# Performance work log

Measured on AMD Instinct MI355X. Metric: run time of the kernel, lower is better.

## Reference

```python
import jax, jax.numpy as jnp
import numpy as np

N_NODES = 100000
N_EDGES = 3200000
N_FEAT = 512
N_GRAPHS = 64
N_EXTRA_LAYERS = 3  # layers 2..4, all 1->1


def setup_inputs() -> dict:
    key = jax.random.key(0)
    ks = jax.random.split(key, 10)
    x = jax.random.normal(ks[0], (N_NODES, N_FEAT), dtype=jnp.float32)
    edge_src = jax.random.randint(ks[1], (N_EDGES,), 0, N_NODES, dtype=jnp.int32)
    edge_dst = jax.random.randint(ks[2], (N_EDGES,), 0, N_NODES, dtype=jnp.int32)
    graph_ids = jnp.sort(jax.random.randint(ks[3], (N_NODES,), 0, N_GRAPHS, dtype=jnp.int32))
    W_neigh0 = jax.random.normal(ks[4], (N_FEAT, 1), dtype=jnp.float32) * 0.05
    W_self0 = jax.random.normal(ks[5], (N_FEAT, 1), dtype=jnp.float32) * 0.05
    b0 = jax.random.normal(ks[6], (1,), dtype=jnp.float32)
    W_neigh_r = jax.random.normal(ks[7], (N_EXTRA_LAYERS, 1, 1), dtype=jnp.float32)
    W_self_r = jax.random.normal(ks[8], (N_EXTRA_LAYERS, 1, 1), dtype=jnp.float32)
    b_r = jax.random.normal(ks[9], (N_EXTRA_LAYERS, 1), dtype=jnp.float32)
    return {"x": x, "edge_src": edge_src, "edge_dst": edge_dst, "graph_ids": graph_ids,
            "W_neigh0": W_neigh0, "W_self0": W_self0, "b0": b0,
            "W_neigh_r": W_neigh_r, "W_self_r": W_self_r, "b_r": b_r}


def _conv_wl(h, edge_src, edge_dst, W_neigh, W_self, b, n_nodes):
    # GraphConv(norm='none'): project first (in >= out here), gather at src, scatter-sum at dst, + bias
    proj = h @ W_neigh                      # [N, out]
    neigh = jax.ops.segment_sum(proj[edge_src], edge_dst, num_segments=n_nodes) + b
    return neigh + h @ W_self               # residual self-loop linear (no bias)


def reference(x, edge_src, edge_dst, graph_ids, W_neigh0, W_self0, b0, W_neigh_r, W_self_r, b_r):
    n = x.shape[0]
    xs = [x]
    h = jax.nn.relu(_conv_wl(x, edge_src, edge_dst, W_neigh0, W_self0, b0, n))
    xs.append(h)
    for i in range(W_neigh_r.shape[0]):
        h = jax.nn.relu(_conv_wl(h, edge_src, edge_dst, W_neigh_r[i], W_self_r[i], b_r[i], n))
        xs.append(h)
    hcat = jnp.concatenate(xs, axis=1)       # [N, F + num_layers] (concat_features=True)
    # dgl.sum_nodes: per-graph sum over the batched graph
    return jax.ops.segment_sum(hcat, graph_ids, num_segments=N_GRAPHS)  # [G, F + L]
```

## Files before the change

kernel.cpp:

```cpp
#include <hip/hip_runtime.h>

#define N_NODES  100000
#define N_EDGES  3200000
#define N_FEAT   512
#define N_GRAPHS 64
#define N_COLS   516
#define NBINS    1563
#define B1       256
#define EPB      (N_EDGES / B1)
#define CCHUNK   16
#define SRC_MASK 0x1FFFF

__global__ __launch_bounds__(256) void find_starts_kernel(
    const int* __restrict__ gid, int* __restrict__ starts)
{
    const int n = blockIdx.x * blockDim.x + threadIdx.x;
    if (n >= N_NODES) return;
    const int g = gid[n];
    const int gp = (n == 0) ? -1 : gid[n - 1];
    for (int q = gp + 1; q <= g; ++q) starts[q] = n;
    if (n == N_NODES - 1)
        for (int q = g + 1; q <= N_GRAPHS; ++q) starts[q] = N_NODES;
}

__global__ __launch_bounds__(256) void dots_kernel(
    const float* __restrict__ x, const float* __restrict__ wn,
    const float* __restrict__ ws, float* __restrict__ p0, float* __restrict__ s0)
{
    const int lane = threadIdx.x & 63;
    const int wid = (blockIdx.x * blockDim.x + threadIdx.x) >> 6;
    const int nwaves = (gridDim.x * blockDim.x) >> 6;

    const float4 wna = *(const float4*)(wn + lane * 8);
    const float4 wnb = *(const float4*)(wn + lane * 8 + 4);
    const float4 wsa = *(const float4*)(ws + lane * 8);
    const float4 wsb = *(const float4*)(ws + lane * 8 + 4);

    for (int n = wid; n < N_NODES; n += nwaves) {
        const float* row = x + (size_t)n * N_FEAT;
        const float4 xa = *(const float4*)(row + lane * 8);
        const float4 xb = *(const float4*)(row + lane * 8 + 4);
        float dn = xa.x*wna.x + xa.y*wna.y + xa.z*wna.z + xa.w*wna.w
                 + xb.x*wnb.x + xb.y*wnb.y + xb.z*wnb.z + xb.w*wnb.w;
        float dv = xa.x*wsa.x + xa.y*wsa.y + xa.z*wsa.z + xa.w*wsa.w
                 + xb.x*wsb.x + xb.y*wsb.y + xb.z*wsb.z + xb.w*wsb.w;
        #pragma unroll
        for (int off = 32; off > 0; off >>= 1) {
            dn += __shfl_down(dn, off);
            dv += __shfl_down(dv, off);
        }
        if (lane == 0) { p0[n] = dn; s0[n] = dv; }
    }
}

__global__ __launch_bounds__(256) void colsum_kernel(
    const float* __restrict__ x, const int* __restrict__ starts,
    float* __restrict__ partial)
{
    const int g = blockIdx.y, chunk = blockIdx.x;
    const int walker = threadIdx.x >> 7;
    const int t = threadIdx.x & 127;
    const int s = starts[g], e = starts[g + 1];
    const int len = e - s;
    const int rs = s + (int)(((long long)len * chunk) / CCHUNK);
    const int re = s + (int)(((long long)len * (chunk + 1)) / CCHUNK);

    float4 acc = make_float4(0.f, 0.f, 0.f, 0.f);
    for (int r = rs + walker; r < re; r += 2) {
        const float4 v = *(const float4*)(x + (size_t)r * N_FEAT + t * 4);
        acc.x += v.x; acc.y += v.y; acc.z += v.z; acc.w += v.w;
    }
    const int slot = chunk * 2 + walker;
    *(float4*)(partial + ((size_t)slot * N_GRAPHS + g) * N_FEAT + t * 4) = acc;
}

__global__ __launch_bounds__(512) void reduce_partial_kernel(
    const float* __restrict__ partial, float* __restrict__ out)
{
    const int g = blockIdx.x, c = threadIdx.x;
    float s = 0.f;
    for (int k = 0; k < 2 * CCHUNK; ++k)
        s += partial[((size_t)k * N_GRAPHS + g) * N_FEAT + c];
    out[(size_t)g * N_COLS + c] = s;
}

__global__ __launch_bounds__(256) void hist_kernel(
    const int* __restrict__ edst, int* __restrict__ histG)
{
    __shared__ int lh[NBINS];
    const int b = blockIdx.x, tid = threadIdx.x;
    for (int i = tid; i < NBINS; i += 256) lh[i] = 0;
    __syncthreads();
    const int e0 = b * EPB;
    for (int e = e0 + tid; e < e0 + EPB; e += 256)
        atomicAdd(&lh[edst[e] >> 6], 1);
    __syncthreads();
    for (int i = tid; i < NBINS; i += 256) histG[i * B1 + b] = lh[i];
}

__global__ __launch_bounds__(256) void colscan_kernel(
    const int* __restrict__ histG, int* __restrict__ colscanG,
    int* __restrict__ totalG)
{
    __shared__ int sc[256];
    const int bin = blockIdx.x, t = threadIdx.x;
    const int v = histG[bin * B1 + t];
    sc[t] = v;
    __syncthreads();
    for (int off = 1; off < 256; off <<= 1) {
        const int a = (t >= off) ? sc[t - off] : 0;
        __syncthreads();
        sc[t] += a;
        __syncthreads();
    }
    colscanG[bin * B1 + t] = sc[t] - v;
    if (t == 255) totalG[bin] = sc[255];
}

__global__ __launch_bounds__(256) void scan2_kernel(
    const int* __restrict__ totalG, int* __restrict__ binstart)
{
    __shared__ int sc[256];
    const int t = threadIdx.x;
    const int CH = 7;
    int loc[CH];
    int s = 0;
    for (int i = 0; i < CH; ++i) {
        const int bin = t * CH + i;
        const int v = (bin < NBINS) ? totalG[bin] : 0;
        loc[i] = s; s += v;
    }
    const int my = s;
    sc[t] = my;
    __syncthreads();
    for (int off = 1; off < 256; off <<= 1) {
        const int a = (t >= off) ? sc[t - off] : 0;
        __syncthreads();
        sc[t] += a;
        __syncthreads();
    }
    const int texcl = sc[t] - my;
    for (int i = 0; i < CH; ++i) {
        const int bin = t * CH + i;
        if (bin < NBINS) binstart[bin] = texcl + loc[i];
    }
    if (t == 255) binstart[NBINS] = sc[255];
}

__global__ __launch_bounds__(256) void reorder_kernel(
    const int* __restrict__ esrc, const int* __restrict__ edst,
    const int* __restrict__ binstart, const int* __restrict__ colscanG,
    int* __restrict__ sorted)
{
    __shared__ int offs[NBINS];
    const int b = blockIdx.x, tid = threadIdx.x;
    for (int i = tid; i < NBINS; i += 256)
        offs[i] = binstart[i] + colscanG[i * B1 + b];
    __syncthreads();
    const int e0 = b * EPB;
    for (int e = e0 + tid; e < e0 + EPB; e += 256) {
        const int s = esrc[e], d = edst[e];
        const int p = atomicAdd(&offs[d >> 6], 1);
        sorted[p] = s | ((d & 63) << 17);
    }
}

__global__ __launch_bounds__(256) void binned_scatter_kernel(
    const int* __restrict__ sorted, const int* __restrict__ binstart,
    const float* __restrict__ pin, const float* __restrict__ self_in,
    const float* __restrict__ wself_p, const float* __restrict__ bias_p,
    const float* __restrict__ wnext_p,
    float* __restrict__ h_out, float* __restrict__ p_next,
    const int* __restrict__ gid, float* __restrict__ out, int col)
{
    __shared__ float acc[4][64];
    const int b = blockIdx.x, tid = threadIdx.x;
    ((float*)acc)[tid] = 0.f;
    __syncthreads();

    const int st = binstart[b], en = binstart[b + 1];
    const int w = tid >> 6;
    for (int e = st + tid; e < en; e += 256) {
        const int v = sorted[e];
        atomicAdd(&acc[w][v >> 17], pin[v & SRC_MASK]);
    }
    __syncthreads();

    if (tid < 64) {
        const int n = b * 64 + tid;
        const bool valid = (n < N_NODES);
        float h = 0.f;
        int g = 0;
        if (valid) {
            const float nb = acc[0][tid] + acc[1][tid] + acc[2][tid] + acc[3][tid];
            const float sw = wself_p ? *wself_p : 1.0f;
            const float v = nb + *bias_p + sw * self_in[n];
            h = v > 0.f ? v : 0.f;
            h_out[n] = h;
            if (wnext_p) p_next[n] = h * (*wnext_p);
            g = gid[n];
        }
        const int g0 = __shfl(g, 0);
        if (__all(!valid || g == g0)) {
            float s = h;
            #pragma unroll
            for (int off = 32; off > 0; off >>= 1) s += __shfl_down(s, off);
            if (tid == 0) atomicAdd(&out[(size_t)g0 * N_COLS + col], s);
        } else if (valid) {
            atomicAdd(&out[(size_t)g * N_COLS + col], h);
        }
    }
}

extern "C" void kernel_launch(void* const* d_in, const int* in_sizes, int n_in,
                              void* d_out, int out_size, void* d_ws, size_t ws_size,
                              hipStream_t stream)
{
    (void)in_sizes; (void)n_in; (void)out_size; (void)ws_size;

    const float* x    = (const float*)d_in[0];
    const int*   esrc = (const int*)d_in[1];
    const int*   edst = (const int*)d_in[2];
    const int*   gid  = (const int*)d_in[3];
    const float* Wn0  = (const float*)d_in[4];
    const float* Ws0  = (const float*)d_in[5];
    const float* b0p  = (const float*)d_in[6];
    const float* Wnr  = (const float*)d_in[7];
    const float* Wsr  = (const float*)d_in[8];
    const float* brp  = (const float*)d_in[9];
    float* out = (float*)d_out;

    float* bufP  = (float*)d_ws;
    float* bufP2 = bufP  + N_NODES;
    float* bufS  = bufP2 + N_NODES;
    float* bufH  = bufS  + N_NODES;
    int*   starts   = (int*)(bufH + N_NODES);
    int*   binstart = starts + (N_GRAPHS + 1);
    int*   totalG   = binstart + NBINS + 1;
    int*   histG    = totalG + NBINS;
    int*   colscanG = histG + (size_t)NBINS * B1;
    int*   sorted   = colscanG + (size_t)NBINS * B1;
    float* partial  = (float*)(sorted + N_EDGES);

    hipMemsetAsync(d_out, 0, (size_t)N_GRAPHS * N_COLS * sizeof(float), stream);

    find_starts_kernel<<<(N_NODES + 255) / 256, 256, 0, stream>>>(gid, starts);
    dots_kernel<<<1024, 256, 0, stream>>>(x, Wn0, Ws0, bufP, bufS);
    colsum_kernel<<<dim3(CCHUNK, N_GRAPHS), 256, 0, stream>>>(x, starts, partial);
    reduce_partial_kernel<<<N_GRAPHS, 512, 0, stream>>>(partial, out);

    hist_kernel<<<B1, 256, 0, stream>>>(edst, histG);
    colscan_kernel<<<NBINS, 256, 0, stream>>>(histG, colscanG, totalG);
    scan2_kernel<<<1, 256, 0, stream>>>(totalG, binstart);
    reorder_kernel<<<B1, 256, 0, stream>>>(esrc, edst, binstart, colscanG, sorted);

    binned_scatter_kernel<<<NBINS, 256, 0, stream>>>(
        sorted, binstart, bufP, bufS, nullptr, b0p, Wnr + 0, bufH, bufP2, gid, out, 512);
    binned_scatter_kernel<<<NBINS, 256, 0, stream>>>(
        sorted, binstart, bufP2, bufH, Wsr + 0, brp + 0, Wnr + 1, bufH, bufP, gid, out, 513);
    binned_scatter_kernel<<<NBINS, 256, 0, stream>>>(
        sorted, binstart, bufP, bufH, Wsr + 1, brp + 1, Wnr + 2, bufH, bufP2, gid, out, 514);
    binned_scatter_kernel<<<NBINS, 256, 0, stream>>>(
        sorted, binstart, bufP2, bufH, Wsr + 2, brp + 2, nullptr, bufH, nullptr, gid, out, 515);
}
```

Baseline: 525.6 us.

## Fuse x dot products with per-graph column sums in one pass over x

```diff
diff --git a/kernel.cpp b/kernel.cpp
--- a/kernel.cpp
+++ b/kernel.cpp
@@ -8,38 +8,93 @@
 #define NBINS    1563
 #define B1       256
 #define EPB      (N_EDGES / B1)
-#define CCHUNK   16
+#define CHUNK    25
+#define NWAVES   (N_NODES / CHUNK)
 #define SRC_MASK 0x1FFFF
 
-__global__ __launch_bounds__(256) void find_starts_kernel(
-    const int* __restrict__ gid, int* __restrict__ starts)
-{
-    const int n = blockIdx.x * blockDim.x + threadIdx.x;
-    if (n >= N_NODES) return;
-    const int g = gid[n];
-    const int gp = (n == 0) ? -1 : gid[n - 1];
-    for (int q = gp + 1; q <= g; ++q) starts[q] = n;
-    if (n == N_NODES - 1)
-        for (int q = g + 1; q <= N_GRAPHS; ++q) starts[q] = N_NODES;
-}
-
-__global__ __launch_bounds__(256) void dots_kernel(
-    const float* __restrict__ x, const float* __restrict__ wn,
-    const float* __restrict__ ws, float* __restrict__ p0, float* __restrict__ s0)
-{
+__global__ __launch_bounds__(1024) void prep_kernel(
+    const int* __restrict__ edst, const int* __restrict__ gid,
+    int* __restrict__ histG, int* __restrict__ starts, float* __restrict__ outz)
+{
+    __shared__ int lh[NBINS];
+    const int b = blockIdx.x, tid = threadIdx.x;
+    const int gtid = b * 1024 + tid;
+
+    if (gtid < N_GRAPHS * N_COLS) outz[gtid] = 0.f;
+    if (gtid < N_NODES) {
+        const int g = gid[gtid];
+        const int gp = gtid ? gid[gtid - 1] : -1;
+        for (int q = gp + 1; q <= g; ++q) starts[q] = gtid;
+        if (gtid == N_NODES - 1)
+            for (int q = g + 1; q <= N_GRAPHS; ++q) starts[q] = N_NODES;
+    }
+    for (int i = tid; i < NBINS; i += 1024) lh[i] = 0;
+    __syncthreads();
+    const int e0 = b * EPB;
+    for (int e = e0 + tid; e < e0 + EPB; e += 1024)
+        atomicAdd(&lh[edst[e] >> 6], 1);
+    __syncthreads();
+    for (int i = tid; i < NBINS; i += 1024) histG[i * B1 + b] = lh[i];
+}
+
+__device__ __forceinline__ void flush_cs(
+    int si, int cur_g, const float a[8], int wave, int lane,
+    float* __restrict__ pp, int* __restrict__ pt, float* __restrict__ out)
+{
+    if (si < 2) {
+        const int slot = wave * 2 + si;
+        if (lane == 0) pt[slot] = cur_g;
+        float* d = pp + (size_t)slot * N_FEAT + lane * 8;
+        *(float4*)d       = make_float4(a[0], a[1], a[2], a[3]);
+        *(float4*)(d + 4) = make_float4(a[4], a[5], a[6], a[7]);
+    } else {
+        float* o = out + (size_t)cur_g * N_COLS + lane * 8;
+        #pragma unroll
+        for (int k = 0; k < 8; ++k) atomicAdd(o + k, a[k]);
+    }
+}
+
+__global__ __launch_bounds__(256) void pass_x_kernel(
+    const float* __restrict__ x, const int* __restrict__ gid,
+    const float* __restrict__ wn, const float* __restrict__ ws,
+    float* __restrict__ p0, float* __restrict__ s0,
+    float* __restrict__ neigh, float* __restrict__ out,
+    float* __restrict__ pp, int* __restrict__ pt)
+{
+    const int wave = (blockIdx.x * blockDim.x + threadIdx.x) >> 6;
     const int lane = threadIdx.x & 63;
-    const int wid = (blockIdx.x * blockDim.x + threadIdx.x) >> 6;
-    const int nwaves = (gridDim.x * blockDim.x) >> 6;
+    const int start = wave * CHUNK, end = start + CHUNK;
+
+    for (int n = start + lane; n < end; n += 64) neigh[n] = 0.f;
 
     const float4 wna = *(const float4*)(wn + lane * 8);
     const float4 wnb = *(const float4*)(wn + lane * 8 + 4);
     const float4 wsa = *(const float4*)(ws + lane * 8);
     const float4 wsb = *(const float4*)(ws + lane * 8 + 4);
 
-    for (int n = wid; n < N_NODES; n += nwaves) {
+    float a[8] = {0.f, 0.f, 0.f, 0.f, 0.f, 0.f, 0.f, 0.f};
+    int cur_g = gid[start];
+    const bool uniform = (gid[end - 1] == cur_g);
+    int si = 0;
+
+    for (int n = start; n < end; ++n) {
+        if (!uniform) {
+            const int g = gid[n];
+            if (g != cur_g) {
+                flush_cs(si, cur_g, a, wave, lane, pp, pt, out);
+                ++si;
+                #pragma unroll
+                for (int k = 0; k < 8; ++k) a[k] = 0.f;
+                cur_g = g;
+            }
+        }
         const float* row = x + (size_t)n * N_FEAT;
         const float4 xa = *(const float4*)(row + lane * 8);
         const float4 xb = *(const float4*)(row + lane * 8 + 4);
+
+        a[0] += xa.x; a[1] += xa.y; a[2] += xa.z; a[3] += xa.w;
+        a[4] += xb.x; a[5] += xb.y; a[6] += xb.z; a[7] += xb.w;
+
         float dn = xa.x*wna.x + xa.y*wna.y + xa.z*wna.z + xa.w*wna.w
                  + xb.x*wnb.x + xb.y*wnb.y + xb.z*wnb.z + xb.w*wnb.w;
         float dv = xa.x*wsa.x + xa.y*wsa.y + xa.z*wsa.z + xa.w*wsa.w
@@ -51,51 +106,30 @@
         }
         if (lane == 0) { p0[n] = dn; s0[n] = dv; }
     }
-}
-
-__global__ __launch_bounds__(256) void colsum_kernel(
-    const float* __restrict__ x, const int* __restrict__ starts,
-    float* __restrict__ partial)
-{
-    const int g = blockIdx.y, chunk = blockIdx.x;
-    const int walker = threadIdx.x >> 7;
-    const int t = threadIdx.x & 127;
+    flush_cs(si, cur_g, a, wave, lane, pp, pt, out);
+    ++si;
+    if (lane == 0)
+        for (int s2 = si; s2 < 2; ++s2) pt[wave * 2 + s2] = -1;
+}
+
+__global__ __launch_bounds__(512) void reduce_x_kernel(
+    const float* __restrict__ pp, const int* __restrict__ pt,
+    const int* __restrict__ starts, float* __restrict__ out)
+{
+    const int g = blockIdx.x, c = threadIdx.x;
     const int s = starts[g], e = starts[g + 1];
-    const int len = e - s;
-    const int rs = s + (int)(((long long)len * chunk) / CCHUNK);
-    const int re = s + (int)(((long long)len * (chunk + 1)) / CCHUNK);
-
-    float4 acc = make_float4(0.f, 0.f, 0.f, 0.f);
-    for (int r = rs + walker; r < re; r += 2) {
-        const float4 v = *(const float4*)(x + (size_t)r * N_FEAT + t * 4);
-        acc.x += v.x; acc.y += v.y; acc.z += v.z; acc.w += v.w;
-    }
-    const int slot = chunk * 2 + walker;
-    *(float4*)(partial + ((size_t)slot * N_GRAPHS + g) * N_FEAT + t * 4) = acc;
-}
-
-__global__ __launch_bounds__(512) void reduce_partial_kernel(
-    const float* __restrict__ partial, float* __restrict__ out)
-{
-    const int g = blockIdx.x, c = threadIdx.x;
-    float s = 0.f;
-    for (int k = 0; k < 2 * CCHUNK; ++k)
-        s += partial[((size_t)k * N_GRAPHS + g) * N_FEAT + c];
-    out[(size_t)g * N_COLS + c] = s;
-}
-
-__global__ __launch_bounds__(256) void hist_kernel(
-    const int* __restrict__ edst, int* __restrict__ histG)
-{
-    __shared__ int lh[NBINS];
-    const int b = blockIdx.x, tid = threadIdx.x;
-    for (int i = tid; i < NBINS; i += 256) lh[i] = 0;
-    __syncthreads();
-    const int e0 = b * EPB;
-    for (int e = e0 + tid; e < e0 + EPB; e += 256)
-        atomicAdd(&lh[edst[e] >> 6], 1);
-    __syncthreads();
-    for (int i = tid; i < NBINS; i += 256) histG[i * B1 + b] = lh[i];
+    float acc = 0.f;
+    if (e > s) {
+        const int w0 = s / CHUNK, w1 = (e - 1) / CHUNK;
+        for (int w = w0; w <= w1; ++w) {
+            #pragma unroll
+            for (int k = 0; k < 2; ++k) {
+                const int slot = w * 2 + k;
+                if (pt[slot] == g) acc += pp[(size_t)slot * N_FEAT + c];
+            }
+        }
+    }
+    out[(size_t)g * N_COLS + c] += acc;
 }
 
 __global__ __launch_bounds__(256) void colscan_kernel(
@@ -147,18 +181,18 @@
     if (t == 255) binstart[NBINS] = sc[255];
 }
 
-__global__ __launch_bounds__(256) void reorder_kernel(
+__global__ __launch_bounds__(1024) void reorder_kernel(
     const int* __restrict__ esrc, const int* __restrict__ edst,
     const int* __restrict__ binstart, const int* __restrict__ colscanG,
     int* __restrict__ sorted)
 {
     __shared__ int offs[NBINS];
     const int b = blockIdx.x, tid = threadIdx.x;
-    for (int i = tid; i < NBINS; i += 256)
+    for (int i = tid; i < NBINS; i += 1024)
         offs[i] = binstart[i] + colscanG[i * B1 + b];
     __syncthreads();
     const int e0 = b * EPB;
-    for (int e = e0 + tid; e < e0 + EPB; e += 256) {
+    for (int e = e0 + tid; e < e0 + EPB; e += 1024) {
         const int s = esrc[e], d = edst[e];
         const int p = atomicAdd(&offs[d >> 6], 1);
         sorted[p] = s | ((d & 63) << 17);
@@ -230,29 +264,27 @@
     const float* brp  = (const float*)d_in[9];
     float* out = (float*)d_out;
 
-    float* bufP  = (float*)d_ws;
+    float* pp    = (float*)d_ws;
+    float* bufP  = pp + (size_t)NWAVES * 2 * N_FEAT;
     float* bufP2 = bufP  + N_NODES;
     float* bufS  = bufP2 + N_NODES;
     float* bufH  = bufS  + N_NODES;
-    int*   starts   = (int*)(bufH + N_NODES);
+    int*   pt       = (int*)(bufH + N_NODES);
+    int*   starts   = pt + NWAVES * 2;
     int*   binstart = starts + (N_GRAPHS + 1);
     int*   totalG   = binstart + NBINS + 1;
     int*   histG    = totalG + NBINS;
     int*   colscanG = histG + (size_t)NBINS * B1;
     int*   sorted   = colscanG + (size_t)NBINS * B1;
-    float* partial  = (float*)(sorted + N_EDGES);
-
-    hipMemsetAsync(d_out, 0, (size_t)N_GRAPHS * N_COLS * sizeof(float), stream);
-
-    find_starts_kernel<<<(N_NODES + 255) / 256, 256, 0, stream>>>(gid, starts);
-    dots_kernel<<<1024, 256, 0, stream>>>(x, Wn0, Ws0, bufP, bufS);
-    colsum_kernel<<<dim3(CCHUNK, N_GRAPHS), 256, 0, stream>>>(x, starts, partial);
-    reduce_partial_kernel<<<N_GRAPHS, 512, 0, stream>>>(partial, out);
-
-    hist_kernel<<<B1, 256, 0, stream>>>(edst, histG);
+
+    prep_kernel<<<B1, 1024, 0, stream>>>(edst, gid, histG, starts, out);
+    pass_x_kernel<<<NWAVES / 4, 256, 0, stream>>>(
+        x, gid, Wn0, Ws0, bufP, bufS, bufP2 ,
+        out, pp, pt);
     colscan_kernel<<<NBINS, 256, 0, stream>>>(histG, colscanG, totalG);
     scan2_kernel<<<1, 256, 0, stream>>>(totalG, binstart);
-    reorder_kernel<<<B1, 256, 0, stream>>>(esrc, edst, binstart, colscanG, sorted);
+    reorder_kernel<<<B1, 1024, 0, stream>>>(esrc, edst, binstart, colscanG, sorted);
+    reduce_x_kernel<<<N_GRAPHS, 512, 0, stream>>>(pp, pt, starts, out);
 
     binned_scatter_kernel<<<NBINS, 256, 0, stream>>>(
         sorted, binstart, bufP, bufS, nullptr, b0p, Wnr + 0, bufH, bufP2, gid, out, 512);
```

Result: faster. 508.5 us (-3.2%).
